# Kernel tuning notes

Measured on AMD Instinct MI355X. Metric: run time of the kernel, lower is better.

## Reference

```python
import jax, jax.numpy as jnp
import numpy as np
from jax import lax
import math

C = 512
B = 8
T = 8192


def _kaiser_sinc_filter1d(cutoff, half_width, kernel_size):
    # exact port of torch kaiser_sinc_filter1d (even kernel branch for k=12)
    half_size = kernel_size // 2
    delta_f = 4.0 * half_width
    A = 2.285 * (half_size - 1) * math.pi * delta_f + 7.95
    if A > 50.0:
        beta = 0.1102 * (A - 8.7)
    elif A >= 21.0:
        beta = 0.5842 * (A - 21.0) ** 0.4 + 0.07886 * (A - 21.0)
    else:
        beta = 0.0
    window = np.kaiser(kernel_size, beta)  # symmetric == torch periodic=False
    if kernel_size % 2 == 0:
        time = np.arange(-half_size, half_size) + 0.5
    else:
        time = np.arange(kernel_size) - half_size
    filt = 2.0 * cutoff * window * np.sinc(2.0 * cutoff * time)
    filt = filt / filt.sum()
    return filt.astype(np.float32)  # [kernel_size]


def _make_up_down_filters(channels, ratio=2, kernel_size=12):
    f = _kaiser_sinc_filter1d(0.5 / ratio, 0.5 / ratio, kernel_size)
    # upsample weight: polyphase split of f*ratio -> [2,1,6], repeat per channel -> [2C,1,6]
    w = f * ratio
    p0, p1 = w[0::2], w[1::2]
    up = np.stack([p0, p1], axis=0)[:, None, :]            # [2,1,6]
    up = np.tile(up, (channels, 1, 1))                     # [2C,1,6]
    # downsample (low-pass) weight: [C,1,12]
    down = np.tile(f.reshape(1, 1, kernel_size), (channels, 1, 1))
    return jnp.asarray(up), jnp.asarray(down)


def _conv1d(x, w, stride=1, padding=0, dilation=1, groups=1):
    return lax.conv_general_dilated(
        x, w, window_strides=(stride,), padding=[(padding, padding)],
        rhs_dilation=(dilation,), dimension_numbers=('NCH', 'OIH', 'NCH'),
        feature_group_count=groups)


def _snake_beta(x, alpha, beta):
    # alpha_logscale=True
    a = jnp.exp(alpha)[None, :, None]
    b = jnp.exp(beta)[None, :, None]
    return x + (1.0 - jnp.cos(2.0 * a * x)) / (2.0 * b + 1e-9)


def _upsample(x, up_filt):
    b, c, _ = x.shape
    xp = jnp.pad(x, ((0, 0), (0, 0), (2, 3)))
    out = _conv1d(xp, up_filt, groups=c)                   # [B, 2C, T']
    out = out.reshape(b, c, 2, -1)                         # (channel, phase) split
    out = jnp.transpose(out, (0, 1, 3, 2)).reshape(b, c, -1)  # interleave phases
    return out[..., 2:-2]                                  # [B, C, 2T-4]


def _downsample(x, down_filt):
    c = x.shape[1]
    return _conv1d(x, down_filt, stride=2, padding=5, groups=c)


def _activation1d(x, alpha, beta, up_filt, down_filt):
    x = _upsample(x, up_filt)
    x = _snake_beta(x, alpha, beta)
    return _downsample(x, down_filt)


def _wn_weight(v, g):
    # weight_norm (dim=0): w = g * v / ||v||, norm over (in, k) per output channel
    norm = jnp.sqrt(jnp.sum(v * v, axis=(1, 2), keepdims=True))
    return g[:, None, None] * v / norm


def setup_inputs() -> dict:
    key = jax.random.key(0)
    ks = jax.random.split(key, 12)
    x = jax.random.normal(ks[0], (B, C, T), dtype=jnp.float32)
    alpha1 = 0.1 * jax.random.normal(ks[1], (C,), dtype=jnp.float32)
    beta1 = 0.1 * jax.random.normal(ks[2], (C,), dtype=jnp.float32)
    alpha2 = 0.1 * jax.random.normal(ks[3], (C,), dtype=jnp.float32)
    beta2 = 0.1 * jax.random.normal(ks[4], (C,), dtype=jnp.float32)
    scale = 1.0 / np.sqrt(C * 3)
    v1 = scale * jax.random.normal(ks[5], (C, C, 3), dtype=jnp.float32)
    g1 = jax.random.uniform(ks[6], (C,), dtype=jnp.float32, minval=0.5, maxval=1.5)
    b1 = 0.01 * jax.random.normal(ks[7], (C,), dtype=jnp.float32)
    v2 = scale * jax.random.normal(ks[8], (C, C, 3), dtype=jnp.float32)
    g2 = jax.random.uniform(ks[9], (C,), dtype=jnp.float32, minval=0.5, maxval=1.5)
    b2 = 0.01 * jax.random.normal(ks[10], (C,), dtype=jnp.float32)
    up_filt, down_filt = _make_up_down_filters(C)
    return dict(x=x, alpha1=alpha1, beta1=beta1, alpha2=alpha2, beta2=beta2,
                v1=v1, g1=g1, b1=b1, v2=v2, g2=g2, b2=b2,
                up_filt=up_filt, down_filt=down_filt)


def reference(x, alpha1, beta1, alpha2, beta2, v1, g1, b1, v2, g2, b2,
              up_filt, down_filt):
    w1 = _wn_weight(v1, g1)
    w2 = _wn_weight(v2, g2)
    # dilation = (1,3,5) -> convs1 uses dilation[0] = 1, padding = get_padding(3,1) = 1
    xt = _activation1d(x, alpha1, beta1, up_filt, down_filt)    # [B,C,T-2]
    xt = _conv1d(xt, w1, padding=1, dilation=1) + b1[None, :, None]
    xt = _activation1d(xt, alpha2, beta2, up_filt, down_filt)   # [B,C,T-4]
    xt = _conv1d(xt, w2, padding=1, dilation=1) + b2[None, :, None]
    x_residual = x[..., :xt.shape[2]]                            # narrow(2, 0, T-4)
    return xt + x_residual
```

## Files before the change

### kernel.cpp

```cpp
#include <hip/hip_runtime.h>
#include <hip/hip_bf16.h>

#define CCH 512
#define BATCH 8
#define TLEN 8192
#define RPITCH ((size_t)TLEN * CCH)

using f32x4 = __attribute__((ext_vector_type(4))) float;
using s16x8 = __attribute__((ext_vector_type(8))) short;
using s16x4 = __attribute__((ext_vector_type(4))) short;
using s16x2 = __attribute__((ext_vector_type(2))) short;

__device__ __forceinline__ float b2f(short s) {
    union { unsigned int i; float f; } u; u.i = ((unsigned int)(unsigned short)s) << 16; return u.f;
}
__device__ __forceinline__ short f2b(float f) {
    __hip_bfloat16 h = __float2bfloat16(f);
    return *reinterpret_cast<short*>(&h);
}

__device__ __forceinline__ void glds16(const void* g, void* l) {
    __builtin_amdgcn_global_load_lds(
        (const __attribute__((address_space(1))) unsigned int*)g,
        (__attribute__((address_space(3))) unsigned int*)l, 16, 0, 0);
}

__global__ __launch_bounds__(256) void wn_pack_kernel(const float* __restrict__ v,
                                                      const float* __restrict__ g,
                                                      short* __restrict__ wp)
{
    int co = blockIdx.x;
    const float* vr = v + (size_t)co * (CCH * 3);
    float s = 0.f;
    for (int i = threadIdx.x; i < CCH * 3; i += 256) { float xv = vr[i]; s += xv * xv; }
#pragma unroll
    for (int off = 32; off > 0; off >>= 1) s += __shfl_down(s, off);
    __shared__ float red[4];
    int lane = threadIdx.x & 63, wv = threadIdx.x >> 6;
    if (lane == 0) red[wv] = s;
    __syncthreads();
    float tot = red[0] + red[1] + red[2] + red[3];
    float scale = g[co] / sqrtf(tot);
    for (int i = threadIdx.x; i < CCH * 3; i += 256) {
        int ci = i / 3, tap = i - ci * 3;
        size_t dst = ((size_t)(((ci >> 5) * 4 + (co >> 7)) * 3 + tap)) * 4096
                     + (size_t)(co & 127) * 32 + (ci & 31);
        wp[dst] = f2b(vr[i] * scale);
    }
}

__global__ __launch_bounds__(256) void transpose_kernel2(const float* __restrict__ x,
                                                         short* __restrict__ out)
{
    __shared__ float ls[64][65];
    int tid = threadIdx.x;
    int t0 = blockIdx.x * 64, c0 = blockIdx.y * 64, b = blockIdx.z;
    const float* xb = x + (size_t)b * CCH * TLEN;
#pragma unroll
    for (int p = 0; p < 4; ++p) {
        int c = p * 16 + (tid >> 4);
        int t4 = (tid & 15) * 4;
        f32x4 v = *(const f32x4*)&xb[(size_t)(c0 + c) * TLEN + t0 + t4];
#pragma unroll
        for (int i = 0; i < 4; ++i) ls[c][t4 + i] = v[i];
    }
    __syncthreads();
    short* ob = out + (size_t)b * RPITCH;
#pragma unroll
    for (int p = 0; p < 4; ++p) {
        int t = p * 16 + (tid >> 4);
        int c4 = (tid & 15) * 4;
        s16x4 o;
#pragma unroll
        for (int i = 0; i < 4; ++i) o[i] = f2b(ls[c4 + i][t]);
        *(s16x4*)(ob + (size_t)(t0 + t) * CCH + c0 + c4) = o;
    }
}

#define ALT 64
__global__ __launch_bounds__(256, 4) void act_kernel(
    const short* __restrict__ in, short* __restrict__ out,
    const float* __restrict__ alpha, const float* __restrict__ beta,
    const float* __restrict__ upf, const float* __restrict__ dwf,
    int Tin, int Tout)
{
    int tid = threadIdx.x;
    int c2 = tid * 2;
    int b = blockIdx.z;
    int t0 = blockIdx.x * ALT;
    const short* ib = in + (size_t)b * RPITCH + c2;
    short* ob = out + (size_t)b * RPITCH + c2;

    float ph0[6], ph1[6], fw[12];
#pragma unroll
    for (int m = 0; m < 6; ++m) { ph0[m] = upf[m]; ph1[m] = upf[6 + m]; }
#pragma unroll
    for (int k = 0; k < 12; ++k) fw[k] = dwf[k];

    float twoa[2], inv2b[2];
#pragma unroll
    for (int ch = 0; ch < 2; ++ch) {
        twoa[ch]  = 2.f * __expf(alpha[c2 + ch]);
        inv2b[ch] = 1.f / (2.f * __expf(beta[c2 + ch]) + 1e-9f);
    }
    int Ls = 2 * Tin - 4;

    auto ldx2 = [&](int t, float* dst) {
        if (t >= 0 && t < Tin) {
            s16x2 v = *(const s16x2*)(ib + (size_t)t * CCH);
            dst[0] = b2f(v[0]); dst[1] = b2f(v[1]);
        } else { dst[0] = 0.f; dst[1] = 0.f; }
    };

    float xa[12][2];
#pragma unroll
    for (int i = 0; i < 12; ++i) ldx2(t0 - 4 + i, xa[i]);
    float sr[12][2];
#pragma unroll
    for (int i = 0; i < 12; ++i) {
        int j = 2 * t0 - 5 + i;
        int xoff = ((i - 3) >> 1) + 2;
        const float* ph = ((i + 1) & 1) ? ph1 : ph0;
        bool ok = (j >= 0 && j < Ls);
#pragma unroll
        for (int ch = 0; ch < 2; ++ch) {
            float u = 0.f;
#pragma unroll
            for (int m = 0; m < 6; ++m) u += ph[m] * xa[xoff + m][ch];
            sr[i][ch] = ok ? (u + (1.f - __cosf(twoa[ch] * u)) * inv2b[ch]) : 0.f;
        }
    }
    float xw[9][2];
#pragma unroll
    for (int m = 0; m < 6; ++m) { xw[m][0] = xa[6 + m][0]; xw[m][1] = xa[6 + m][1]; }
    ldx2(t0 + 8,  xw[6]);
    ldx2(t0 + 9,  xw[7]);
    ldx2(t0 + 10, xw[8]);

#pragma unroll 4
    for (int it = 0; it < ALT; ++it) {
        int t = t0 + it;
        float y[2] = {0.f, 0.f};
#pragma unroll
        for (int k = 0; k < 12; ++k) {
            y[0] += fw[k] * sr[k][0];
            y[1] += fw[k] * sr[k][1];
        }
        if (t < Tout) {
            s16x2 o; o[0] = f2b(y[0]); o[1] = f2b(y[1]);
            *(s16x2*)(ob + (size_t)t * CCH) = o;
        }
        bool ok1 = (2 * t + 7 < Ls), ok2 = (2 * t + 8 < Ls);
        float s1[2], s2[2];
#pragma unroll
        for (int ch = 0; ch < 2; ++ch) {
            float u1 = 0.f, u2 = 0.f;
#pragma unroll
            for (int m = 0; m < 6; ++m) {
                u1 += ph1[m] * xw[m][ch];
                u2 += ph0[m] * xw[m + 1][ch];
            }
            s1[ch] = ok1 ? (u1 + (1.f - __cosf(twoa[ch] * u1)) * inv2b[ch]) : 0.f;
            s2[ch] = ok2 ? (u2 + (1.f - __cosf(twoa[ch] * u2)) * inv2b[ch]) : 0.f;
        }
#pragma unroll
        for (int i = 0; i < 10; ++i) { sr[i][0] = sr[i + 2][0]; sr[i][1] = sr[i + 2][1]; }
        sr[10][0] = s1[0]; sr[10][1] = s1[1];
        sr[11][0] = s2[0]; sr[11][1] = s2[1];
#pragma unroll
        for (int m = 0; m < 8; ++m) { xw[m][0] = xw[m + 1][0]; xw[m][1] = xw[m + 1][1]; }
        ldx2(t + 11, xw[8]);
    }
}

template <int MODE>
__global__ __launch_bounds__(256, 2) void conv_mfma(
    const short* __restrict__ xin, const short* __restrict__ wp,
    const float* __restrict__ bias, const float* __restrict__ resid,
    float* __restrict__ outF, short* __restrict__ outT, int rows)
{
    constexpr int IB = 132 * 32;
    __shared__ __align__(16) short lds[17408];

    int tid = threadIdx.x;
    int wave = tid >> 6, lane = tid & 63;
    int quad = lane >> 4, l16 = lane & 15;
    int wm = wave >> 1, wn = wave & 1;
    int bx = blockIdx.x;
    int cog = bx & 3, tt = bx >> 2;
    int t0 = tt * 128, b = blockIdx.z;

    const short* inb = xin + (size_t)b * RPITCH;
    bool interior = (t0 >= 1) && (t0 + 129 <= rows);

    auto stage = [&](int cc, int pbuf) {
        short* il = lds + pbuf * IB;
        const short* isrc = inb + (size_t)(t0 - 1) * CCH + cc * 32;
        if (interior) {
#pragma unroll
            for (int p = 0; p < 2; ++p) {
                int seg0 = (p * 4 + wave) * 64;
                int s = seg0 + lane;
                int u = s ^ ((s >> 3) & 3);
                glds16(isrc + (size_t)(u >> 2) * CCH + (u & 3) * 8, il + seg0 * 8);
            }
            if (wave == 0 && lane < 8) {
                int s = 512 + lane;
                glds16(isrc + (size_t)(s >> 2) * CCH + (s & 3) * 8, il + 512 * 8);
            }
        } else {
            for (int s = tid; s < 520; s += 256) {
                int gt = t0 - 1 + (s >> 2);
                s16x8 v = 0;
                if (gt >= 0 && gt < rows)
                    v = *(const s16x8*)(inb + (size_t)gt * CCH + cc * 32 + (s & 3) * 8);
                int ps = s ^ ((s >> 3) & 3);
                *(s16x8*)(il + ps * 8) = v;
            }
        }
    };

    const short* wbase = wp + (size_t)(wm * 64 + l16) * 32 + quad * 8;
    auto loadA = [&](int cc, s16x8 (&ar)[3][4]) {
        const short* wc = wbase + (size_t)((cc * 4 + cog) * 3) * 4096;
#pragma unroll
        for (int tap = 0; tap < 3; ++tap)
#pragma unroll
            for (int mf = 0; mf < 4; ++mf)
                ar[tap][mf] = *(const s16x8*)(wc + tap * 4096 + mf * 512);
    };

    f32x4 acc[4][4];
#pragma unroll
    for (int i = 0; i < 4; ++i)
#pragma unroll
        for (int j = 0; j < 4; ++j) acc[i][j] = 0.f;

    auto compute = [&](const s16x8 (&ar)[3][4], const short* il) {
#pragma unroll
        for (int tap = 0; tap < 3; ++tap) {
            s16x8 bv[4];
#pragma unroll
            for (int nf = 0; nf < 4; ++nf) {
                int row = wn * 64 + nf * 16 + l16 + tap;
                int off = (quad * 8) ^ (((row >> 1) & 3) << 3);
                bv[nf] = *(const s16x8*)(il + row * 32 + off);
            }
#pragma unroll
            for (int mf = 0; mf < 4; ++mf)
#pragma unroll
                for (int nf = 0; nf < 4; ++nf)
                    acc[mf][nf] = __builtin_amdgcn_mfma_f32_16x16x32_bf16(
                        ar[tap][mf], bv[nf], acc[mf][nf], 0, 0, 0);
        }
    };

    s16x8 a0[3][4], a1[3][4];
    loadA(0, a0);
    loadA(1, a1);
    stage(0, 0);
    __syncthreads();

    for (int cc2 = 0; cc2 < 8; ++cc2) {
        int ccA = 2 * cc2;
        stage(ccA + 1, 1);
        compute(a0, lds);
        if (ccA + 2 < 16) loadA(ccA + 2, a0);
        __syncthreads();
        if (ccA + 2 < 16) stage(ccA + 2, 0);
        compute(a1, lds + IB);
        if (ccA + 3 < 16) loadA(ccA + 3, a1);
        __syncthreads();
    }

    f32x4 b4[4];
#pragma unroll
    for (int mf = 0; mf < 4; ++mf)
        b4[mf] = *(const f32x4*)(bias + cog * 128 + wm * 64 + mf * 16 + quad * 4);

    if (MODE == 0) {
        short* ot = lds;
#pragma unroll
        for (int mf = 0; mf < 4; ++mf)
#pragma unroll
            for (int nf = 0; nf < 4; ++nf) {
                int t = wn * 64 + nf * 16 + l16;
                int co = wm * 64 + mf * 16 + quad * 4;
                s16x4 o;
#pragma unroll
                for (int r = 0; r < 4; ++r) o[r] = f2b(acc[mf][nf][r] + b4[mf][r]);
                *(s16x4*)(ot + t * 136 + co) = o;
            }
        __syncthreads();
#pragma unroll
        for (int rr = 0; rr < 8; ++rr) {
            int idx = rr * 256 + tid;
            int tr = idx >> 4, c8 = (idx & 15) * 8;
            int t = t0 + tr;
            if (t < rows)
                *(s16x8*)(outT + (size_t)b * RPITCH + (size_t)t * CCH + cog * 128 + c8)
                    = *(const s16x8*)(ot + tr * 136 + c8);
        }
    } else {
        float* of = (float*)lds;
#pragma unroll
        for (int h = 0; h < 2; ++h) {
            if (wm == h) {
#pragma unroll
                for (int mf = 0; mf < 4; ++mf)
#pragma unroll
                    for (int nf = 0; nf < 4; ++nf) {
                        int t = wn * 64 + nf * 16 + l16;
#pragma unroll
                        for (int r = 0; r < 4; ++r)
                            of[(mf * 16 + quad * 4 + r) * 132 + t] = acc[mf][nf][r] + b4[mf][r];
                    }
            }
            __syncthreads();
#pragma unroll
            for (int rr = 0; rr < 8; ++rr) {
                int idx = rr * 256 + tid;
                int row = idx >> 5, c4 = (idx & 31) * 4;
                int co = cog * 128 + h * 64 + row;
                int t = t0 + c4;
                f32x4 v = *(const f32x4*)(of + row * 132 + c4);
                size_t ro = (size_t)b * CCH + co;
                const float* rrow = resid + ro * TLEN;
                float* orow = outF + ro * (size_t)rows;
                if (t + 3 < rows) {
                    f32x4 rv = *(const f32x4*)(rrow + t);
                    f32x4 ov;
#pragma unroll
                    for (int i = 0; i < 4; ++i) ov[i] = v[i] + rv[i];
                    *(f32x4*)(orow + t) = ov;
                } else {
#pragma unroll
                    for (int i = 0; i < 4; ++i)
                        if (t + i < rows) orow[t + i] = v[i] + rrow[t + i];
                }
            }
            __syncthreads();
        }
    }
}

extern "C" void kernel_launch(void* const* d_in, const int* in_sizes, int n_in,
                              void* d_out, int out_size, void* d_ws, size_t ws_size,
                              hipStream_t stream)
{
    const float* x      = (const float*)d_in[0];
    const float* alpha1 = (const float*)d_in[1];
    const float* beta1  = (const float*)d_in[2];
    const float* alpha2 = (const float*)d_in[3];
    const float* beta2  = (const float*)d_in[4];
    const float* v1     = (const float*)d_in[5];
    const float* g1     = (const float*)d_in[6];
    const float* b1     = (const float*)d_in[7];
    const float* v2     = (const float*)d_in[8];
    const float* g2     = (const float*)d_in[9];
    const float* b2     = (const float*)d_in[10];
    const float* upf    = (const float*)d_in[11];
    const float* dwf    = (const float*)d_in[12];
    float* out = (float*)d_out;

    const int T1 = TLEN - 2;
    const int T2 = TLEN - 4;

    char* wsb = (char*)d_ws;
    short* w1p = (short*)wsb;
    short* w2p = w1p + (size_t)CCH * CCH * 3;
    short* bufX = w2p + (size_t)CCH * CCH * 3;
    short* bufY = bufX + (size_t)BATCH * RPITCH;

    wn_pack_kernel<<<CCH, 256, 0, stream>>>(v1, g1, w1p);
    wn_pack_kernel<<<CCH, 256, 0, stream>>>(v2, g2, w2p);

    transpose_kernel2<<<dim3(TLEN / 64, CCH / 64, BATCH), 256, 0, stream>>>(x, bufX);

    act_kernel<<<dim3((TLEN + ALT - 1) / ALT, 1, BATCH), 256, 0, stream>>>(
        bufX, bufY, alpha1, beta1, upf, dwf, TLEN, T1);

    conv_mfma<0><<<dim3(256, 1, BATCH), 256, 0, stream>>>(
        bufY, w1p, b1, nullptr, nullptr, bufX, T1);

    act_kernel<<<dim3((T1 + ALT - 1) / ALT, 1, BATCH), 256, 0, stream>>>(
        bufX, bufY, alpha2, beta2, upf, dwf, T1, T2);

    conv_mfma<1><<<dim3(256, 1, BATCH), 256, 0, stream>>>(
        bufY, w2p, b2, x, out, nullptr, T2);
}
```

Measured before the change: 700.2 us.

## Replace direct global-to-LDS loads with register-staged pipeline in conv_mfma

The conv MFMA kernel stops using global_load_lds for input tiles. It now loads the next input chunk into registers, runs the MFMAs on the current LDS buffer, then writes the registers to the other LDS buffer, with one barrier per chunk instead of the two-chunk unrolled loop. Weights now use a single register set instead of double-buffered A registers. The launch-bounds occupancy hint is dropped and s_setprio raises priority around the MFMA block. The aim is fewer barriers and better overlap of loads with compute, at the cost of possibly exposing weight-load latency and changing register pressure and occupancy.

```diff
diff --git a/kernel.cpp b/kernel.cpp
--- a/kernel.cpp
+++ b/kernel.cpp
@@ -17,12 +17,6 @@
 __device__ __forceinline__ short f2b(float f) {
     __hip_bfloat16 h = __float2bfloat16(f);
     return *reinterpret_cast<short*>(&h);
-}
-
-__device__ __forceinline__ void glds16(const void* g, void* l) {
-    __builtin_amdgcn_global_load_lds(
-        (const __attribute__((address_space(1))) unsigned int*)g,
-        (__attribute__((address_space(3))) unsigned int*)l, 16, 0, 0);
 }
 
 __global__ __launch_bounds__(256) void wn_pack_kernel(const float* __restrict__ v,
@@ -174,7 +168,7 @@
 }
 
 template <int MODE>
-__global__ __launch_bounds__(256, 2) void conv_mfma(
+__global__ __launch_bounds__(256) void conv_mfma(
     const short* __restrict__ xin, const short* __restrict__ wp,
     const float* __restrict__ bias, const float* __restrict__ resid,
     float* __restrict__ outF, short* __restrict__ outT, int rows)
@@ -193,41 +187,50 @@
     const short* inb = xin + (size_t)b * RPITCH;
     bool interior = (t0 >= 1) && (t0 + 129 <= rows);
 
-    auto stage = [&](int cc, int pbuf) {
-        short* il = lds + pbuf * IB;
+    int s0 = wave * 64 + lane;
+    int s1 = (4 + wave) * 64 + lane;
+    int s2 = 512 + lane;
+    bool tail = (wave == 0) && (lane < 8);
+
+    s16x8 ir0, ir1, ir2;
+    auto iload = [&](int cc) {
         const short* isrc = inb + (size_t)(t0 - 1) * CCH + cc * 32;
         if (interior) {
-#pragma unroll
-            for (int p = 0; p < 2; ++p) {
-                int seg0 = (p * 4 + wave) * 64;
-                int s = seg0 + lane;
-                int u = s ^ ((s >> 3) & 3);
-                glds16(isrc + (size_t)(u >> 2) * CCH + (u & 3) * 8, il + seg0 * 8);
-            }
-            if (wave == 0 && lane < 8) {
-                int s = 512 + lane;
-                glds16(isrc + (size_t)(s >> 2) * CCH + (s & 3) * 8, il + 512 * 8);
-            }
+            ir0 = *(const s16x8*)(isrc + (size_t)(s0 >> 2) * CCH + (s0 & 3) * 8);
+            ir1 = *(const s16x8*)(isrc + (size_t)(s1 >> 2) * CCH + (s1 & 3) * 8);
+            if (tail)
+                ir2 = *(const s16x8*)(isrc + (size_t)(s2 >> 2) * CCH + (s2 & 3) * 8);
         } else {
-            for (int s = tid; s < 520; s += 256) {
-                int gt = t0 - 1 + (s >> 2);
-                s16x8 v = 0;
-                if (gt >= 0 && gt < rows)
-                    v = *(const s16x8*)(inb + (size_t)gt * CCH + cc * 32 + (s & 3) * 8);
-                int ps = s ^ ((s >> 3) & 3);
-                *(s16x8*)(il + ps * 8) = v;
-            }
-        }
+            int gt0 = t0 - 1 + (s0 >> 2);
+            int gt1 = t0 - 1 + (s1 >> 2);
+            ir0 = 0; ir1 = 0; ir2 = 0;
+            if (gt0 >= 0 && gt0 < rows)
+                ir0 = *(const s16x8*)(inb + (size_t)gt0 * CCH + cc * 32 + (s0 & 3) * 8);
+            if (gt1 >= 0 && gt1 < rows)
+                ir1 = *(const s16x8*)(inb + (size_t)gt1 * CCH + cc * 32 + (s1 & 3) * 8);
+            if (tail) {
+                int gt2 = t0 - 1 + (s2 >> 2);
+                if (gt2 >= 0 && gt2 < rows)
+                    ir2 = *(const s16x8*)(inb + (size_t)gt2 * CCH + cc * 32 + (s2 & 3) * 8);
+            }
+        }
+    };
+    auto iwrite = [&](int pbuf) {
+        short* il = lds + pbuf * IB;
+        *(s16x8*)(il + (s0 ^ ((s0 >> 3) & 3)) * 8) = ir0;
+        *(s16x8*)(il + (s1 ^ ((s1 >> 3) & 3)) * 8) = ir1;
+        if (tail) *(s16x8*)(il + s2 * 8) = ir2;
     };
 
     const short* wbase = wp + (size_t)(wm * 64 + l16) * 32 + quad * 8;
-    auto loadA = [&](int cc, s16x8 (&ar)[3][4]) {
+    s16x8 areg[3][4];
+    auto loadA = [&](int cc) {
         const short* wc = wbase + (size_t)((cc * 4 + cog) * 3) * 4096;
 #pragma unroll
         for (int tap = 0; tap < 3; ++tap)
 #pragma unroll
             for (int mf = 0; mf < 4; ++mf)
-                ar[tap][mf] = *(const s16x8*)(wc + tap * 4096 + mf * 512);
+                areg[tap][mf] = *(const s16x8*)(wc + tap * 4096 + mf * 512);
     };
 
     f32x4 acc[4][4];
@@ -236,7 +239,9 @@
 #pragma unroll
         for (int j = 0; j < 4; ++j) acc[i][j] = 0.f;
 
-    auto compute = [&](const s16x8 (&ar)[3][4], const short* il) {
+    auto compute = [&](int pbuf) {
+        const short* il = lds + pbuf * IB;
+        __builtin_amdgcn_s_setprio(1);
 #pragma unroll
         for (int tap = 0; tap < 3; ++tap) {
             s16x8 bv[4];
@@ -251,26 +256,28 @@
 #pragma unroll
                 for (int nf = 0; nf < 4; ++nf)
                     acc[mf][nf] = __builtin_amdgcn_mfma_f32_16x16x32_bf16(
-                        ar[tap][mf], bv[nf], acc[mf][nf], 0, 0, 0);
-        }
-    };
-
-    s16x8 a0[3][4], a1[3][4];
-    loadA(0, a0);
-    loadA(1, a1);
-    stage(0, 0);
-    __syncthreads();
-
-    for (int cc2 = 0; cc2 < 8; ++cc2) {
-        int ccA = 2 * cc2;
-        stage(ccA + 1, 1);
-        compute(a0, lds);
-        if (ccA + 2 < 16) loadA(ccA + 2, a0);
-        __syncthreads();
-        if (ccA + 2 < 16) stage(ccA + 2, 0);
-        compute(a1, lds + IB);
-        if (ccA + 3 < 16) loadA(ccA + 3, a1);
-        __syncthreads();
+                        areg[tap][mf], bv[nf], acc[mf][nf], 0, 0, 0);
+        }
+        __builtin_amdgcn_s_setprio(0);
+    };
+
+    iload(0);
+    loadA(0);
+    iwrite(0);
+    asm volatile("s_waitcnt lgkmcnt(0)" ::: "memory");
+    __builtin_amdgcn_sched_barrier(0);
+    __builtin_amdgcn_s_barrier();
+
+    for (int cc = 0; cc < 16; ++cc) {
+        if (cc < 15) iload(cc + 1);
+        compute(cc & 1);
+        if (cc < 15) {
+            loadA(cc + 1);
+            iwrite((cc + 1) & 1);
+        }
+        asm volatile("s_waitcnt lgkmcnt(0)" ::: "memory");
+        __builtin_amdgcn_sched_barrier(0);
+        __builtin_amdgcn_s_barrier();
     }
 
     f32x4 b4[4];
```

Result: faster. 664.7 us (-5.1%).
